# Performance work log

Measured on AMD Instinct MI355X. Metric: run time of the kernel, lower is better.

The kernel has to match this reference:

```python
import jax, jax.numpy as jnp
import numpy as np
import math

D_MODEL = 1024
NUM_HEADS = 16
N_GROUP = 4
HEAD_DIM = D_MODEL // NUM_HEADS  # 64
KV_DIM = N_GROUP * HEAD_DIM      # 256
BS, SEQ = 2, 2048


def setup_inputs() -> dict:
    key = jax.random.key(0)
    ks = jax.random.split(key, 7)
    s = 0.02
    return {
        "h": jax.random.normal(ks[0], (BS, SEQ, D_MODEL), dtype=jnp.float32),
        "wq_w": jax.random.normal(ks[1], (D_MODEL, D_MODEL), dtype=jnp.float32) * s,
        "wq_b": jnp.zeros((D_MODEL,), dtype=jnp.float32),
        "wk_w": jax.random.normal(ks[2], (KV_DIM, D_MODEL), dtype=jnp.float32) * s,
        "wk_b": jnp.zeros((KV_DIM,), dtype=jnp.float32),
        "wv_w": jax.random.normal(ks[3], (KV_DIM, D_MODEL), dtype=jnp.float32) * s,
        "wv_b": jnp.zeros((KV_DIM,), dtype=jnp.float32),
    }


def reference(h, wq_w, wq_b, wk_w, wk_b, wv_w, wv_b):
    bs, seq, _ = h.shape
    rep = NUM_HEADS // N_GROUP  # heads per KV group

    # Linear projections (torch Linear: x @ W.T + b)
    q = h @ wq_w.T + wq_b                     # [bs, seq, d_model]
    k = h @ wk_w.T + wk_b                     # [bs, seq, kv_dim]
    v = h @ wv_w.T + wv_b                     # [bs, seq, kv_dim]

    q = q.reshape(bs, seq, NUM_HEADS, HEAD_DIM).transpose(0, 2, 1, 3)  # [b,H,s,d]
    k = k.reshape(bs, seq, N_GROUP, HEAD_DIM)                          # [b,s,G,d]
    v = v.reshape(bs, seq, N_GROUP, HEAD_DIM)
    # torch .repeat(1,1,1,rep).view(...,num_heads,head_dim) maps head h -> group h//rep,
    # identical to repeating each group `rep` times consecutively along the head axis.
    k = jnp.repeat(k, rep, axis=2).transpose(0, 2, 1, 3)               # [b,H,s,d]
    v = jnp.repeat(v, rep, axis=2).transpose(0, 2, 1, 3)               # [b,H,s,d]

    scores = jnp.einsum("bhqd,bhkd->bhqk", q, k) / math.sqrt(HEAD_DIM)
    attn = jax.nn.softmax(scores, axis=-1)
    out = jnp.einsum("bhqk,bhkd->bhqd", attn, v)                       # [b,H,s,d]
    out = out.transpose(0, 2, 1, 3).reshape(bs, seq, NUM_HEADS * HEAD_DIM)
    return out
```

## Files before the change

### kernel.cpp

```cpp
#include <hip/hip_runtime.h>

typedef _Float16 f16;
typedef _Float16 f16x8 __attribute__((ext_vector_type(8)));
typedef _Float16 f16x4 __attribute__((ext_vector_type(4)));
typedef float f32x4 __attribute__((ext_vector_type(4)));

#define MFMA16(a, b, c)   __builtin_amdgcn_mfma_f32_16x16x32_f16((a), (b), (c), 0, 0, 0)
#define MFMA16K(a, b, c)  __builtin_amdgcn_mfma_f32_16x16x16f16((a), (b), (c), 0, 0, 0)

#define SEQ 2048
#define DMODEL 1024
#define NH 16
#define NG 4
#define PAD 76

__device__ __forceinline__ f16x8 cvt8(const float4 a, const float4 b) {
    f16x8 r;
    r[0] = (f16)a.x; r[1] = (f16)a.y; r[2] = (f16)a.z; r[3] = (f16)a.w;
    r[4] = (f16)b.x; r[5] = (f16)b.y; r[6] = (f16)b.z; r[7] = (f16)b.w;
    return r;
}

__device__ __forceinline__ void gl_lds16(f16* lds, const f16* g) {
    __builtin_amdgcn_global_load_lds(
        (const __attribute__((address_space(1))) void*)g,
        (__attribute__((address_space(3))) void*)lds, 16, 0, 0);
}

#define HN  (4096 * 1024)
#define WQN (1024 * 1024)
#define WKN (256 * 1024)
#define WVN (256 * 1024)
#define TOT8 ((HN + WQN + WKN + WVN) / 8)

__global__ __launch_bounds__(256) void cvt_kernel(const float* __restrict__ h,
                                                  const float* __restrict__ wq,
                                                  const float* __restrict__ wk,
                                                  const float* __restrict__ wv,
                                                  f16* __restrict__ h16,
                                                  f16* __restrict__ W16) {
    const int c = blockIdx.x * 256 + threadIdx.x;
    if (c >= TOT8) return;
    const size_t e = (size_t)c * 8;
    const float* src;
    f16* dst;
    if (e < HN) {
        src = h + e; dst = h16 + e;
    } else {
        const size_t e2 = e - HN;
        if (e2 < WQN)            src = wq + e2;
        else if (e2 < WQN + WKN) src = wk + (e2 - WQN);
        else                     src = wv + (e2 - WQN - WKN);
        dst = W16 + e2;
    }
    const float4 a = *(const float4*)src;
    const float4 b = *(const float4*)(src + 4);
    *(f16x8*)dst = cvt8(a, b);
}

__global__ __launch_bounds__(256, 3) void qkv_gemm16(const f16* __restrict__ A,
                                                     const f16* __restrict__ W,
                                                     const float* __restrict__ bq,
                                                     const float* __restrict__ bk,
                                                     const float* __restrict__ bv,
                                                     f16* __restrict__ Qb,
                                                     f16* __restrict__ Kb,
                                                     f16* __restrict__ Vtb,
                                                     float qscale) {
    __shared__ __align__(16) f16 As[2][64 * 32];
    __shared__ __align__(16) f16 Bs[2][128 * 32];

    const int tid  = threadIdx.x;
    const int lane = tid & 63;
    const int l15  = lane & 15;
    const int l4   = lane >> 4;
    const int wave = tid >> 6;
    const int wm   = (wave >> 1) * 32;
    const int wn   = (wave & 1) * 64;
    const int bx   = blockIdx.x;
    const int m0   = blockIdx.y * 64;
    const int n0g  = bx * 128;

    const f16* Ag = A + ((size_t)(m0 + (lane >> 2))) * 1024 + (lane & 3) * 8;
    const f16* Wg = W + ((size_t)(n0g + (lane >> 2))) * 1024 + (lane & 3) * 8;
    const size_t rstep = (size_t)16 * 1024;

    f32x4 acc[2][4];
#pragma unroll
    for (int i = 0; i < 2; i++)
#pragma unroll
        for (int j = 0; j < 4; j++) acc[i][j] = (f32x4)0.0f;

    gl_lds16(&As[0][wave * 512],        Ag + (size_t)wave * rstep);
    gl_lds16(&Bs[0][wave * 1024],       Wg + (size_t)(wave * 2) * rstep);
    gl_lds16(&Bs[0][wave * 1024 + 512], Wg + (size_t)(wave * 2 + 1) * rstep);

    int cur = 0;
    for (int k0 = 0; k0 < DMODEL; k0 += 32) {
        __syncthreads();
        if (k0 + 32 < DMODEL) {
            const int nxt = cur ^ 1;
            const int kn = k0 + 32;
            gl_lds16(&As[nxt][wave * 512],        Ag + (size_t)wave * rstep + kn);
            gl_lds16(&Bs[nxt][wave * 1024],       Wg + (size_t)(wave * 2) * rstep + kn);
            gl_lds16(&Bs[nxt][wave * 1024 + 512], Wg + (size_t)(wave * 2 + 1) * rstep + kn);
        }

        const f16* Ab = As[cur];
        const f16* Bb = Bs[cur];
        f16x8 af[2], bf[4];
#pragma unroll
        for (int i = 0; i < 2; i++)
            af[i] = *(const f16x8*)&Ab[(wm + i * 16 + l15) * 32 + l4 * 8];
#pragma unroll
        for (int j = 0; j < 4; j++)
            bf[j] = *(const f16x8*)&Bb[(wn + j * 16 + l15) * 32 + l4 * 8];
        __builtin_amdgcn_s_setprio(1);
#pragma unroll
        for (int i = 0; i < 2; i++)
#pragma unroll
            for (int j = 0; j < 4; j++)
                acc[i][j] = MFMA16(af[i], bf[j], acc[i][j]);
        __builtin_amdgcn_s_setprio(0);
        cur ^= 1;
    }

    const float* bias; f16* C; int N, n0; float osc; int vmode;
    if (bx < 8)       { bias = bq; C = Qb;  N = 1024; n0 = bx * 128;        osc = qscale; vmode = 0; }
    else if (bx < 10) { bias = bk; C = Kb;  N = 256;  n0 = (bx - 8) * 128;  osc = 1.0f;   vmode = 0; }
    else              { bias = bv; C = Vtb; N = 256;  n0 = (bx - 10) * 128; osc = 1.0f;   vmode = 1; }

#pragma unroll
    for (int i = 0; i < 2; i++) {
        const int mbase = m0 + wm + i * 16 + l4 * 4;
#pragma unroll
        for (int j = 0; j < 4; j++) {
            const int n  = n0 + wn + j * 16 + l15;
            const float bb = bias[n];
            if (vmode == 0) {
#pragma unroll
                for (int r = 0; r < 4; r++)
                    C[(size_t)(mbase + r) * N + n] = (f16)((acc[i][j][r] + bb) * osc);
            } else {
                f16x4 p;
#pragma unroll
                for (int r = 0; r < 4; r++)
                    p[r] = (f16)((acc[i][j][r] + bb) * osc);
                const int batch = mbase >> 11;
                const int s     = mbase & 2047;
                *(f16x4*)&C[((size_t)(batch * 256 + n)) * SEQ + s] = p;
            }
        }
    }
}

__global__ __launch_bounds__(256, 3) void attn_kernel(const f16* __restrict__ Q,
                                                      const f16* __restrict__ Kt,
                                                      const f16* __restrict__ Vt,
                                                      float* __restrict__ out) {
    __shared__ __align__(16) f16 KV[2][2][2][64][32];
    float* Scr = (float*)&KV[0][0][0][0][0];
    float* Lr  = (float*)((char*)&KV[0][0][0][0][0] + 24576);

    const int tid  = threadIdx.x;
    const int lane = tid & 63;
    const int l15  = lane & 15;
    const int l4   = lane >> 4;
    const int w    = tid >> 6;
    const int b    = blockIdx.z;
    const int hh   = blockIdx.y;
    const int g    = hh >> 2;
    const int q0   = blockIdx.x * 64;

    f16x8 qf[4][2];
#pragma unroll
    for (int rg = 0; rg < 4; rg++)
#pragma unroll
        for (int kt = 0; kt < 2; kt++)
            qf[rg][kt] = *(const f16x8*)&Q[((size_t)(b * SEQ + q0 + rg * 16 + l15)) * DMODEL
                                           + hh * 64 + kt * 32 + l4 * 8];

    f32x4 oacc[4][4];
    float lsum[4] = {0.0f, 0.0f, 0.0f, 0.0f};
#pragma unroll
    for (int rg = 0; rg < 4; rg++)
#pragma unroll
        for (int dt = 0; dt < 4; dt++) oacc[rg][dt] = (f32x4)0.0f;

    const int gr = lane >> 2;
    const int gc = (lane & 3) * 8;
    const f16* Kg = Kt + ((size_t)(b * SEQ + w * 16 + gr)) * 256 + g * 64 + gc;
    const f16* Vg = Vt + ((size_t)(b * 256 + g * 64 + w * 16 + gr)) * SEQ + gc;

#define STAGE(buf, kb)                                                          \
    do {                                                                        \
        gl_lds16(&KV[buf][0][0][w * 16][0], Kg + (size_t)(kb) * 256);           \
        gl_lds16(&KV[buf][0][1][w * 16][0], Kg + (size_t)(kb) * 256 + 32);      \
        gl_lds16(&KV[buf][1][0][w * 16][0], Vg + (kb));                         \
        gl_lds16(&KV[buf][1][1][w * 16][0], Vg + (kb) + 32);                    \
    } while (0)

    STAGE(0, 0);
    __syncthreads();

    int cur = 0;
    for (int t = 0; t < 32; t++) {
        if (t < 31) STAGE(cur ^ 1, (t + 1) * 64);

        const f16x8 kf0 = *(const f16x8*)&KV[cur][0][0][w * 16 + l15][l4 * 8];
        const f16x8 kf1 = *(const f16x8*)&KV[cur][0][1][w * 16 + l15][l4 * 8];

        f32x4 sacc[4];
#pragma unroll
        for (int rg = 0; rg < 4; rg++) sacc[rg] = (f32x4)0.0f;
#pragma unroll
        for (int rg = 0; rg < 4; rg++) {
            sacc[rg] = MFMA16(kf0, qf[rg][0], sacc[rg]);
            sacc[rg] = MFMA16(kf1, qf[rg][1], sacc[rg]);
        }

        f16x4 pa[4];
#pragma unroll
        for (int rg = 0; rg < 4; rg++)
#pragma unroll
            for (int r = 0; r < 4; r++) {
                const float p = exp2f(fminf(sacc[rg][r], 14.0f));
                lsum[rg] += p;
                pa[rg][r] = (f16)p;
            }

#pragma unroll
        for (int dt = 0; dt < 4; dt++) {
            const f16x4 vf = *(const f16x4*)&KV[cur][1][w >> 1][dt * 16 + l15][(w & 1) * 16 + l4 * 4];
#pragma unroll
            for (int rg = 0; rg < 4; rg++)
                oacc[rg][dt] = MFMA16K(pa[rg], vf, oacc[rg][dt]);
        }

        __syncthreads();
        cur ^= 1;
    }

#pragma unroll
    for (int rg = 0; rg < 4; rg++) {
        lsum[rg] += __shfl_xor(lsum[rg], 16);
        lsum[rg] += __shfl_xor(lsum[rg], 32);
    }
    if (l4 == 0) {
#pragma unroll
        for (int rg = 0; rg < 4; rg++)
            Lr[w * 64 + rg * 16 + l15] = lsum[rg];
    }
    __syncthreads();
    float ltot[4];
#pragma unroll
    for (int rg = 0; rg < 4; rg++)
        ltot[rg] = Lr[0 * 64 + rg * 16 + l15] + Lr[1 * 64 + rg * 16 + l15]
                 + Lr[2 * 64 + rg * 16 + l15] + Lr[3 * 64 + rg * 16 + l15];

    for (int h = 0; h < 2; h++) {
        __syncthreads();
        if (w > 0) {
#pragma unroll
            for (int rgl = 0; rgl < 2; rgl++) {
                const int rg = h * 2 + rgl;
#pragma unroll
                for (int dt = 0; dt < 4; dt++)
#pragma unroll
                    for (int r = 0; r < 4; r++)
                        Scr[((size_t)(w - 1) * 32 + rgl * 16 + l4 * 4 + r) * 64 + dt * 16 + l15]
                            = oacc[rg][dt][r];
            }
        }
        __syncthreads();
        if (w == 0) {
#pragma unroll
            for (int rgl = 0; rgl < 2; rgl++) {
                const int rg = h * 2 + rgl;
#pragma unroll
                for (int r = 0; r < 4; r++) {
                    const float lv  = __shfl(ltot[rg], l4 * 4 + r);
                    const float inv = 1.0f / lv;
                    const int q = q0 + rg * 16 + l4 * 4 + r;
                    float* op = out + ((size_t)(b * SEQ + q)) * DMODEL + hh * 64;
#pragma unroll
                    for (int dt = 0; dt < 4; dt++) {
                        const size_t si = ((size_t)0 * 32 + rgl * 16 + l4 * 4 + r) * 64 + dt * 16 + l15;
                        const float v = oacc[rg][dt][r]
                                      + Scr[si]
                                      + Scr[si + (size_t)32 * 64]
                                      + Scr[si + (size_t)64 * 64];
                        op[dt * 16 + l15] = v * inv;
                    }
                }
            }
        }
    }
#undef STAGE
}

extern "C" void kernel_launch(void* const* d_in, const int* in_sizes, int n_in,
                              void* d_out, int out_size, void* d_ws, size_t ws_size,
                              hipStream_t stream) {
    const float* h    = (const float*)d_in[0];
    const float* wq_w = (const float*)d_in[1];
    const float* wq_b = (const float*)d_in[2];
    const float* wk_w = (const float*)d_in[3];
    const float* wk_b = (const float*)d_in[4];
    const float* wv_w = (const float*)d_in[5];
    const float* wv_b = (const float*)d_in[6];
    float* out = (float*)d_out;

    char* ws = (char*)d_ws;
    f16* Qb  = (f16*)(ws + 0);
    f16* Kb  = (f16*)(ws + 8388608);
    f16* Vtb = (f16*)(ws + 10485760);
    f16* h16 = (f16*)(ws + 12582912);
    f16* W16 = (f16*)(ws + 20971520);

    const float qscale = 0.125f * 1.4426950408889634f;

    cvt_kernel<<<dim3(TOT8 / 256), 256, 0, stream>>>(h, wq_w, wk_w, wv_w, h16, W16);
    qkv_gemm16<<<dim3(12, 64), 256, 0, stream>>>(h16, W16, wq_b, wk_b, wv_b,
                                                 Qb, Kb, Vtb, qscale);
    attn_kernel<<<dim3(32, 16, 2), 256, 0, stream>>>(Qb, Kb, Vtb, out);
}
```

Baseline: 183.9 us.

## Replace async LDS loads with register-staged padded K/V tiles and rotate epilogue reduction

Drops the direct global-to-LDS async loads and instead prefetches the next K/V tile into registers, writing it into padded LDS buffers (row stride PAD) after the current tile's MFMAs. The padding is meant to reduce LDS bank conflicts on fragment reads. The epilogue reduction now rotates which wave reduces each row group, so all waves share the final output writes instead of wave 0 doing all of them. The trade-offs are extra registers for the prefetched data, which may lower occupancy, and more barriers in the epilogue. Scratch aliasing also changes: Scr now sits in Ks and Lr in Vs.

Measured after the change: 179.5 us. -2.4%, faster.

```diff
diff --git a/kernel.cpp b/kernel.cpp
--- a/kernel.cpp
+++ b/kernel.cpp
@@ -158,9 +158,10 @@
                                                       const f16* __restrict__ Kt,
                                                       const f16* __restrict__ Vt,
                                                       float* __restrict__ out) {
-    __shared__ __align__(16) f16 KV[2][2][2][64][32];
-    float* Scr = (float*)&KV[0][0][0][0][0];
-    float* Lr  = (float*)((char*)&KV[0][0][0][0][0] + 24576);
+    __shared__ __align__(16) f16 Ks[2][64 * PAD];
+    __shared__ __align__(16) f16 Vs[2][64 * PAD];
+    float* Scr = (float*)&Ks[0][0];
+    float* Lr  = (float*)&Vs[0][0];
 
     const int tid  = threadIdx.x;
     const int lane = tid & 63;
@@ -187,28 +188,38 @@
 #pragma unroll
         for (int dt = 0; dt < 4; dt++) oacc[rg][dt] = (f32x4)0.0f;
 
-    const int gr = lane >> 2;
-    const int gc = (lane & 3) * 8;
-    const f16* Kg = Kt + ((size_t)(b * SEQ + w * 16 + gr)) * 256 + g * 64 + gc;
-    const f16* Vg = Vt + ((size_t)(b * 256 + g * 64 + w * 16 + gr)) * SEQ + gc;
-
-#define STAGE(buf, kb)                                                          \
-    do {                                                                        \
-        gl_lds16(&KV[buf][0][0][w * 16][0], Kg + (size_t)(kb) * 256);           \
-        gl_lds16(&KV[buf][0][1][w * 16][0], Kg + (size_t)(kb) * 256 + 32);      \
-        gl_lds16(&KV[buf][1][0][w * 16][0], Vg + (kb));                         \
-        gl_lds16(&KV[buf][1][1][w * 16][0], Vg + (kb) + 32);                    \
-    } while (0)
-
-    STAGE(0, 0);
+    const int srow = tid >> 2;
+    const int sc8  = (tid & 3) * 8;
+    const f16* Kg = Kt + (size_t)(b * SEQ + srow) * 256 + g * 64 + sc8;
+    const f16* Vg = Vt + (size_t)(b * 256 + g * 64 + srow) * SEQ + sc8;
+
+    {
+        const f16x8 k0 = *(const f16x8*)(Kg);
+        const f16x8 k1 = *(const f16x8*)(Kg + 32);
+        const f16x8 v0 = *(const f16x8*)(Vg);
+        const f16x8 v1 = *(const f16x8*)(Vg + 32);
+        *(f16x8*)&Ks[0][srow * PAD + sc8]      = k0;
+        *(f16x8*)&Ks[0][srow * PAD + 32 + sc8] = k1;
+        *(f16x8*)&Vs[0][srow * PAD + sc8]      = v0;
+        *(f16x8*)&Vs[0][srow * PAD + 32 + sc8] = v1;
+    }
     __syncthreads();
 
     int cur = 0;
     for (int t = 0; t < 32; t++) {
-        if (t < 31) STAGE(cur ^ 1, (t + 1) * 64);
-
-        const f16x8 kf0 = *(const f16x8*)&KV[cur][0][0][w * 16 + l15][l4 * 8];
-        const f16x8 kf1 = *(const f16x8*)&KV[cur][0][1][w * 16 + l15][l4 * 8];
+        const int kb   = t * 64;
+        const bool more = t < 31;
+
+        f16x8 rk0, rk1, rv0, rv1;
+        if (more) {
+            rk0 = *(const f16x8*)(Kg + (size_t)(kb + 64) * 256);
+            rk1 = *(const f16x8*)(Kg + (size_t)(kb + 64) * 256 + 32);
+            rv0 = *(const f16x8*)(Vg + kb + 64);
+            rv1 = *(const f16x8*)(Vg + kb + 64 + 32);
+        }
+
+        const f16x8 kf0 = *(const f16x8*)&Ks[cur][(w * 16 + l15) * PAD + l4 * 8];
+        const f16x8 kf1 = *(const f16x8*)&Ks[cur][(w * 16 + l15) * PAD + 32 + l4 * 8];
 
         f32x4 sacc[4];
 #pragma unroll
@@ -231,12 +242,19 @@
 
 #pragma unroll
         for (int dt = 0; dt < 4; dt++) {
-            const f16x4 vf = *(const f16x4*)&KV[cur][1][w >> 1][dt * 16 + l15][(w & 1) * 16 + l4 * 4];
+            const f16x4 vf = *(const f16x4*)&Vs[cur][(dt * 16 + l15) * PAD + w * 16 + l4 * 4];
 #pragma unroll
             for (int rg = 0; rg < 4; rg++)
                 oacc[rg][dt] = MFMA16K(pa[rg], vf, oacc[rg][dt]);
         }
 
+        if (more) {
+            const int nxt = cur ^ 1;
+            *(f16x8*)&Ks[nxt][srow * PAD + sc8]      = rk0;
+            *(f16x8*)&Ks[nxt][srow * PAD + 32 + sc8] = rk1;
+            *(f16x8*)&Vs[nxt][srow * PAD + sc8]      = rv0;
+            *(f16x8*)&Vs[nxt][srow * PAD + 32 + sc8] = rv1;
+        }
         __syncthreads();
         cur ^= 1;
     }
@@ -258,45 +276,37 @@
         ltot[rg] = Lr[0 * 64 + rg * 16 + l15] + Lr[1 * 64 + rg * 16 + l15]
                  + Lr[2 * 64 + rg * 16 + l15] + Lr[3 * 64 + rg * 16 + l15];
 
-    for (int h = 0; h < 2; h++) {
+#pragma unroll
+    for (int rg = 0; rg < 4; rg++) {
+        if (w != rg) {
+            const int widx = (w < rg) ? w : w - 1;
+#pragma unroll
+            for (int dt = 0; dt < 4; dt++)
+#pragma unroll
+                for (int r = 0; r < 4; r++)
+                    Scr[((size_t)widx * 16 + l4 * 4 + r) * 64 + dt * 16 + l15] = oacc[rg][dt][r];
+        }
         __syncthreads();
-        if (w > 0) {
-#pragma unroll
-            for (int rgl = 0; rgl < 2; rgl++) {
-                const int rg = h * 2 + rgl;
-#pragma unroll
-                for (int dt = 0; dt < 4; dt++)
-#pragma unroll
-                    for (int r = 0; r < 4; r++)
-                        Scr[((size_t)(w - 1) * 32 + rgl * 16 + l4 * 4 + r) * 64 + dt * 16 + l15]
-                            = oacc[rg][dt][r];
-            }
-        }
-        __syncthreads();
-        if (w == 0) {
-#pragma unroll
-            for (int rgl = 0; rgl < 2; rgl++) {
-                const int rg = h * 2 + rgl;
-#pragma unroll
-                for (int r = 0; r < 4; r++) {
-                    const float lv  = __shfl(ltot[rg], l4 * 4 + r);
-                    const float inv = 1.0f / lv;
-                    const int q = q0 + rg * 16 + l4 * 4 + r;
-                    float* op = out + ((size_t)(b * SEQ + q)) * DMODEL + hh * 64;
-#pragma unroll
-                    for (int dt = 0; dt < 4; dt++) {
-                        const size_t si = ((size_t)0 * 32 + rgl * 16 + l4 * 4 + r) * 64 + dt * 16 + l15;
-                        const float v = oacc[rg][dt][r]
-                                      + Scr[si]
-                                      + Scr[si + (size_t)32 * 64]
-                                      + Scr[si + (size_t)64 * 64];
-                        op[dt * 16 + l15] = v * inv;
-                    }
+        if (w == rg) {
+#pragma unroll
+            for (int r = 0; r < 4; r++) {
+                const float lv  = __shfl(ltot[rg], l4 * 4 + r);
+                const float inv = 1.0f / lv;
+                const int q = q0 + rg * 16 + l4 * 4 + r;
+                float* op = out + ((size_t)(b * SEQ + q)) * DMODEL + hh * 64;
+#pragma unroll
+                for (int dt = 0; dt < 4; dt++) {
+                    const size_t si = ((size_t)(l4 * 4 + r)) * 64 + dt * 16 + l15;
+                    const float v = oacc[rg][dt][r]
+                                  + Scr[si]
+                                  + Scr[si + (size_t)16 * 64]
+                                  + Scr[si + (size_t)32 * 64];
+                    op[dt * 16 + l15] = v * inv;
                 }
             }
         }
-    }
-#undef STAGE
+        __syncthreads();
+    }
 }
 
 extern "C" void kernel_launch(void* const* d_in, const int* in_sizes, int n_in,
```
